# Performance work log

Hardware: AMD Instinct MI355X
Metric: run time of the kernel (lower is better)

## Reference

```python
import jax, jax.numpy as jnp
import numpy as np

N = 20000          # nodes (= masked tokens M, node_ids = arange)
E = 320000         # edges
D_H = 256          # hidden_channels
D_Z = 256          # node_channels
D_A = 256          # attn_channels
D_M = 256          # mlp_hidden_channels
V = 512            # predictor vocab size


def setup_inputs() -> dict:
    key = jax.random.key(0)
    ks = jax.random.split(key, 10)

    def lin(k, fan_in, fan_out):
        return jax.random.normal(k, (fan_in, fan_out), jnp.float32) / np.sqrt(fan_in)

    h_mask = jax.random.normal(ks[0], (N, D_H), jnp.float32)
    z = jax.random.normal(ks[1], (N, D_Z), jnp.float32)
    edge_index = jax.random.randint(ks[2], (2, E), 0, N, dtype=jnp.int32)
    node_ids = jnp.arange(N, dtype=jnp.int32)
    # Pairing of (masked token, edge): with node_ids = arange(N), every edge's
    # dst is a masked node, so masked_idx = dst and edge_idx = arange(E).
    masked_idx = edge_index[1]
    edge_idx = jnp.arange(E, dtype=jnp.int32)
    return {
        "h_mask": h_mask,
        "z": z,
        "Wq": lin(ks[3], D_Z, D_A), "bq": jnp.zeros((D_A,), jnp.float32),
        "Wk": lin(ks[4], D_Z, D_A), "bk": jnp.zeros((D_A,), jnp.float32),
        "W1": lin(ks[5], D_Z, D_M), "b1": jnp.zeros((D_M,), jnp.float32),
        "W2": lin(ks[6], D_M, D_H), "b2": jnp.zeros((D_H,), jnp.float32),
        "Wpred": lin(ks[7], D_H, V), "bpred": jnp.zeros((V,), jnp.float32),
        "edge_index": edge_index,
        "node_ids": node_ids,
        "masked_idx": masked_idx,
        "edge_idx": edge_idx,
    }


def reference(h_mask, z, Wq, bq, Wk, bk, W1, b1, W2, b2, Wpred, bpred,
              edge_index, node_ids, masked_idx, edge_idx):
    src = edge_index[0]
    # Node-level projections (N x D), computed once then gathered per pair.
    q = z @ Wq + bq                      # [N, D_A]
    k = z @ Wk + bk                      # [N, D_A]

    center_nodes = jnp.take(node_ids, masked_idx, axis=0)   # [P]
    neighbor_nodes = jnp.take(src, edge_idx, axis=0)        # [P]

    q_i = jnp.take(q, center_nodes, axis=0)                 # [P, D_A]
    k_j = jnp.take(k, neighbor_nodes, axis=0)               # [P, D_A]
    a_ij = jax.nn.sigmoid(jnp.sum(q_i * k_j, axis=-1, keepdims=True))  # [P, 1]

    h_i = jnp.take(h_mask, masked_idx, axis=0)              # [P, D_H]
    z_j = jnp.take(z, neighbor_nodes, axis=0)               # [P, D_Z]
    g_zj = jax.nn.relu(z_j @ W1 + b1) @ W2 + b2             # [P, D_H]

    h_tilde = a_ij * h_i + (1.0 - a_ij) * g_zj              # [P, D_H]
    edge_logits = h_tilde @ Wpred + bpred                   # [P, V]
    return edge_logits, masked_idx
```

## Files before the change

### kernel.cpp

```cpp
#include <hip/hip_runtime.h>
#include <hip/hip_bf16.h>

typedef __attribute__((ext_vector_type(8))) short s16x8;
typedef __attribute__((ext_vector_type(4))) float f32x4;
typedef __attribute__((ext_vector_type(2))) float f32x2;

__device__ inline unsigned int f2bf(float f) {
    union { float f; unsigned int i; } v;
    v.f = f;
    return (v.i + 0x7FFFu + ((v.i >> 16) & 1u)) >> 16;
}
__device__ inline unsigned char f2fp8(float v) {
    const int p = __builtin_amdgcn_cvt_pk_fp8_f32(v, v, 0, false);
    return (unsigned char)(p & 0xFF);
}

__global__ __launch_bounds__(256) void prep_w(
    const float* __restrict__ Wq, const float* __restrict__ Wk,
    const float* __restrict__ W1, const float* __restrict__ W2,
    const float* __restrict__ Wp,
    const float* __restrict__ bq, const float* __restrict__ bk,
    const float* __restrict__ b1,
    unsigned short* __restrict__ Wtqkt, unsigned short* __restrict__ Wt2,
    unsigned short* __restrict__ Wtp, float* __restrict__ bqkt)
{
    const int tid = threadIdx.x;
    int b = blockIdx.x;
    if (b < 1024) {
        const int w = b >> 8;
        const int i = (b & 255) * 256 + tid;
        const int k = i >> 8, j = i & 255;
        const float* W = (w == 0) ? Wq : (w == 1) ? Wk : (w == 2) ? W1 : W2;
        unsigned short* dst = (w == 3) ? Wt2 : (Wtqkt + w * 65536);
        dst[j * 256 + k] = (unsigned short)f2bf(W[i]);
        return;
    }
    b -= 1024;
    if (b < 512) {
        const int i = b * 256 + tid;
        const int k = i >> 9, j = i & 511;
        Wtp[(size_t)j * 256 + k] = (unsigned short)f2bf(Wp[i]);
        return;
    }
    b -= 512;
    {
        const int i = b * 256 + tid;
        bqkt[i] = (i < 256) ? bq[i] : (i < 512) ? bk[i - 256] : b1[i - 512];
    }
}

struct GemmJob {
    const void* A;
    const unsigned short* Wt;
    const float* bias;
    void* out1;
    void* out2;
    int Nout;
    int split;
    int relu_lo, relu_hi;
    int a_f32;
    int fp8_1, fp8_2;
};

__device__ inline void job_store(const GemmJob& J, int row, int col, float v, int M) {
    if (row >= M) return;
    if (J.bias) v += J.bias[col];
    if (col >= J.relu_lo && col < J.relu_hi) v = fmaxf(v, 0.0f);
    const bool lo = (col < J.split);
    void* o = lo ? J.out1 : J.out2;
    const int stride = lo ? J.split : (J.Nout - J.split);
    const int cc = lo ? col : col - J.split;
    const int f8 = lo ? J.fp8_1 : J.fp8_2;
    if (f8) ((unsigned char*)o)[(size_t)row * stride + cc] = f2fp8(v);
    else    ((unsigned short*)o)[(size_t)row * stride + cc] = (unsigned short)f2bf(v);
}

__global__ __launch_bounds__(256) void gemm_multi(
    GemmJob j0, GemmJob j1, int M)
{
    __shared__ __align__(16) char smem[65536];
    char* ldsA = smem;
    char* ldsB = smem + 32768;
    const GemmJob J = (blockIdx.y == 0) ? j0 : j1;

    const int tid  = threadIdx.x;
    const int wid  = tid >> 6, lane = tid & 63;
    const int wr   = wid >> 1, wc = wid & 1;
    const int r0   = blockIdx.x * 64;
    const int swz  = (lane & 7) << 4;

    if (J.a_f32) {
        const float* Af = (const float*)J.A;
        for (int i = tid; i < 2048; i += 256) {
            const int row = i >> 5, off = i & 31;
            const int gr = r0 + row;
            uint4 v = make_uint4(0, 0, 0, 0);
            if (gr < M) {
                const float4 a = *(const float4*)(Af + (size_t)gr * 256 + off * 8);
                const float4 c = *(const float4*)(Af + (size_t)gr * 256 + off * 8 + 4);
                v.x = f2bf(a.x) | (f2bf(a.y) << 16);
                v.y = f2bf(a.z) | (f2bf(a.w) << 16);
                v.z = f2bf(c.x) | (f2bf(c.y) << 16);
                v.w = f2bf(c.z) | (f2bf(c.w) << 16);
            }
            const int b = (row * 512 + off * 16) ^ ((row & 7) << 4);
            *(uint4*)(ldsA + b) = v;
        }
    } else {
        const unsigned short* Ab = (const unsigned short*)J.A;
        for (int i = tid; i < 2048; i += 256) {
            const int row = i >> 5, off = i & 31;
            const int gr = r0 + row;
            uint4 v = make_uint4(0, 0, 0, 0);
            if (gr < M) v = *(const uint4*)(Ab + (size_t)gr * 256 + off * 8);
            const int b = (row * 512 + off * 16) ^ ((row & 7) << 4);
            *(uint4*)(ldsA + b) = v;
        }
    }

    const int ro = lane & 15, ko = (lane >> 4) * 16;
    const int baseA0 = (wr * 32 +  0 + ro) * 512 + ko;
    const int baseA1 = (wr * 32 + 16 + ro) * 512 + ko;
    const int baseB0 = (wc * 32 +  0 + ro) * 512 + ko;
    const int baseB1 = (wc * 32 + 16 + ro) * 512 + ko;

    const int nchunks = J.Nout >> 6;
    for (int c = 0; c < nchunks; ++c) {
        const int j0c = c << 6;
        for (int i = tid; i < 2048; i += 256) {
            const int row = i >> 5, off = i & 31;
            const uint4 v = *(const uint4*)(J.Wt + (size_t)(j0c + row) * 256 + off * 8);
            const int b = (row * 512 + off * 16) ^ ((row & 7) << 4);
            *(uint4*)(ldsB + b) = v;
        }
        __syncthreads();

        f32x4 acc00 = {0,0,0,0}, acc01 = {0,0,0,0}, acc10 = {0,0,0,0}, acc11 = {0,0,0,0};
#pragma unroll
        for (int kk = 0; kk < 8; ++kk) {
            const int kb = kk * 64;
            const s16x8 a0 = *(const s16x8*)(ldsA + ((baseA0 + kb) ^ swz));
            const s16x8 a1 = *(const s16x8*)(ldsA + ((baseA1 + kb) ^ swz));
            const s16x8 b0 = *(const s16x8*)(ldsB + ((baseB0 + kb) ^ swz));
            const s16x8 b1 = *(const s16x8*)(ldsB + ((baseB1 + kb) ^ swz));
            acc00 = __builtin_amdgcn_mfma_f32_16x16x32_bf16(a0, b0, acc00, 0, 0, 0);
            acc01 = __builtin_amdgcn_mfma_f32_16x16x32_bf16(a0, b1, acc01, 0, 0, 0);
            acc10 = __builtin_amdgcn_mfma_f32_16x16x32_bf16(a1, b0, acc10, 0, 0, 0);
            acc11 = __builtin_amdgcn_mfma_f32_16x16x32_bf16(a1, b1, acc11, 0, 0, 0);
        }

        const int colb = j0c + wc * 32;
        const int rb0 = r0 + wr * 32 + (lane >> 4) * 4;
        const int rb1 = rb0 + 16;
#pragma unroll
        for (int r = 0; r < 4; ++r) {
            job_store(J, rb0 + r, colb + ro,      acc00[r], M);
            job_store(J, rb0 + r, colb + 16 + ro, acc01[r], M);
            job_store(J, rb1 + r, colb + ro,      acc10[r], M);
            job_store(J, rb1 + r, colb + 16 + ro, acc11[r], M);
        }
        __syncthreads();
    }
}

__global__ __launch_bounds__(256) void edge_fused(
    const unsigned char* __restrict__ qkb,
    const unsigned char* __restrict__ hp, const unsigned char* __restrict__ gp,
    const float* __restrict__ bpred,
    const int* __restrict__ edge_src, const int* __restrict__ node_ids,
    const int* __restrict__ masked_idx, const int* __restrict__ edge_idx,
    float* __restrict__ out, int P)
{
    const int wave = threadIdx.x >> 6;
    const int lane = threadIdx.x & 63;
    const int e = blockIdx.x * 4 + wave;
    if (e >= P) return;

    const int mi = masked_idx[e];
    const int c  = node_ids[mi];
    const int s  = edge_src[edge_idx[e]];

    const unsigned int qw = *(const unsigned int*)(qkb + (size_t)c * 512 + lane * 4);
    const unsigned int kw = *(const unsigned int*)(qkb + (size_t)s * 512 + 256 + lane * 4);
    const f32x2 q01 = __builtin_amdgcn_cvt_pk_f32_fp8(qw, false);
    const f32x2 q23 = __builtin_amdgcn_cvt_pk_f32_fp8(qw, true);
    const f32x2 k01 = __builtin_amdgcn_cvt_pk_f32_fp8(kw, false);
    const f32x2 k23 = __builtin_amdgcn_cvt_pk_f32_fp8(kw, true);
    float dot = q01.x * k01.x + q01.y * k01.y + q23.x * k23.x + q23.y * k23.y;
#pragma unroll
    for (int off = 32; off; off >>= 1) dot += __shfl_xor(dot, off, 64);

    const float a = 1.0f / (1.0f + expf(-dot));
    const float oma = 1.0f - a;

    const uint2 hv = *(const uint2*)(hp + (size_t)c * 512 + lane * 8);
    const uint2 gv = *(const uint2*)(gp + (size_t)s * 512 + lane * 8);
    const float4 bp0 = *(const float4*)&bpred[lane * 8];
    const float4 bp1 = *(const float4*)&bpred[lane * 8 + 4];

    const f32x2 h0 = __builtin_amdgcn_cvt_pk_f32_fp8(hv.x, false);
    const f32x2 h1 = __builtin_amdgcn_cvt_pk_f32_fp8(hv.x, true);
    const f32x2 h2 = __builtin_amdgcn_cvt_pk_f32_fp8(hv.y, false);
    const f32x2 h3 = __builtin_amdgcn_cvt_pk_f32_fp8(hv.y, true);
    const f32x2 g0 = __builtin_amdgcn_cvt_pk_f32_fp8(gv.x, false);
    const f32x2 g1 = __builtin_amdgcn_cvt_pk_f32_fp8(gv.x, true);
    const f32x2 g2 = __builtin_amdgcn_cvt_pk_f32_fp8(gv.y, false);
    const f32x2 g3 = __builtin_amdgcn_cvt_pk_f32_fp8(gv.y, true);

    float4 r0, r1;
    r0.x = fmaf(a, h0.x, fmaf(oma, g0.x, bp0.x));
    r0.y = fmaf(a, h0.y, fmaf(oma, g0.y, bp0.y));
    r0.z = fmaf(a, h1.x, fmaf(oma, g1.x, bp0.z));
    r0.w = fmaf(a, h1.y, fmaf(oma, g1.y, bp0.w));
    r1.x = fmaf(a, h2.x, fmaf(oma, g2.x, bp1.x));
    r1.y = fmaf(a, h2.y, fmaf(oma, g2.y, bp1.y));
    r1.z = fmaf(a, h3.x, fmaf(oma, g3.x, bp1.z));
    r1.w = fmaf(a, h3.y, fmaf(oma, g3.y, bp1.w));

    float* dst = &out[(size_t)e * 512 + lane * 8];
    *(float4*)(dst)     = r0;
    *(float4*)(dst + 4) = r1;

    if (lane == 0) {
        out[(size_t)P * 512 + e] = (float)mi;
    }
}

extern "C" void kernel_launch(void* const* d_in, const int* in_sizes, int n_in,
                              void* d_out, int out_size, void* d_ws, size_t ws_size,
                              hipStream_t stream) {
    const float* h_mask = (const float*)d_in[0];
    const float* z      = (const float*)d_in[1];
    const float* Wq     = (const float*)d_in[2];
    const float* bq     = (const float*)d_in[3];
    const float* Wk     = (const float*)d_in[4];
    const float* bk     = (const float*)d_in[5];
    const float* W1     = (const float*)d_in[6];
    const float* b1     = (const float*)d_in[7];
    const float* W2     = (const float*)d_in[8];
    const float* b2     = (const float*)d_in[9];
    const float* Wpred  = (const float*)d_in[10];
    const float* bpred  = (const float*)d_in[11];
    const int* edge_index = (const int*)d_in[12];
    const int* node_ids   = (const int*)d_in[13];
    const int* masked_idx = (const int*)d_in[14];
    const int* edge_idx   = (const int*)d_in[15];

    const int N = in_sizes[13];
    const int P = in_sizes[14];

    unsigned char*  qkb   = (unsigned char*)d_ws;
    unsigned char*  gpb   = qkb + (size_t)N * 512;
    unsigned char*  hpb   = gpb + (size_t)N * 512;
    unsigned short* tb    = (unsigned short*)(hpb + (size_t)N * 512);
    unsigned short* gb    = tb  + (size_t)N * 256;
    unsigned short* Wtqkt = gb  + (size_t)N * 256;
    unsigned short* Wt2   = Wtqkt + 196608;
    unsigned short* Wtp   = Wt2   + 65536;
    float*          bqkt  = (float*)(Wtp + 131072);

    const dim3 blk(256);
    const int gb64 = (N + 63) / 64;
    const int eb   = (P + 3) / 4;

    prep_w<<<dim3(1024 + 512 + 3), blk, 0, stream>>>(
        Wq, Wk, W1, W2, Wpred, bq, bk, b1, Wtqkt, Wt2, Wtp, bqkt);

    GemmJob a0 = { z,      Wtqkt, bqkt,    qkb, tb,      768, 512, 512, 768, 1, 1, 0 };
    GemmJob a1 = { h_mask, Wtp,   nullptr, hpb, nullptr, 512, 512, 0,   0,   1, 1, 0 };
    gemm_multi<<<dim3(gb64, 2), blk, 0, stream>>>(a0, a1, N);

    GemmJob b0 = { tb, Wt2, b2, gb, nullptr, 256, 256, 0, 0, 0, 0, 0 };
    gemm_multi<<<dim3(gb64, 1), blk, 0, stream>>>(b0, b0, N);

    GemmJob c0 = { gb, Wtp, nullptr, gpb, nullptr, 512, 512, 0, 0, 0, 1, 0 };
    gemm_multi<<<dim3(gb64, 1), blk, 0, stream>>>(c0, c0, N);

    edge_fused<<<dim3(eb), blk, 0, stream>>>(qkb, hpb, gpb, bpred,
                                             edge_index, node_ids, masked_idx, edge_idx,
                                             (float*)d_out, P);
}
```

Measured before the change: 349.4 us.

## Process 64 edges per wave with double-buffered gathers and nontemporal stores

The edge kernel now gives each wave a run of 64 edges instead of one. Indices are loaded once per lane and broadcast with shuffles, and the gather loads for the next edge are issued before the current edge is computed, so two edges are in flight. Output stores use nontemporal hints, and the masked_idx tail is written coalesced. The launch has 64x fewer blocks, which lowers occupancy and memory-level parallelism on the store-bound output path.

```diff
diff --git a/kernel.cpp b/kernel.cpp
--- a/kernel.cpp
+++ b/kernel.cpp
@@ -163,7 +163,7 @@
     }
 }
 
-__global__ __launch_bounds__(256) void edge_fused(
+__global__ __launch_bounds__(256) void edge_fused_v2(
     const unsigned char* __restrict__ qkb,
     const unsigned char* __restrict__ hp, const unsigned char* __restrict__ gp,
     const float* __restrict__ bpred,
@@ -171,58 +171,81 @@
     const int* __restrict__ masked_idx, const int* __restrict__ edge_idx,
     float* __restrict__ out, int P)
 {
-    const int wave = threadIdx.x >> 6;
-    const int lane = threadIdx.x & 63;
-    const int e = blockIdx.x * 4 + wave;
-    if (e >= P) return;
-
-    const int mi = masked_idx[e];
-    const int c  = node_ids[mi];
-    const int s  = edge_src[edge_idx[e]];
-
-    const unsigned int qw = *(const unsigned int*)(qkb + (size_t)c * 512 + lane * 4);
-    const unsigned int kw = *(const unsigned int*)(qkb + (size_t)s * 512 + 256 + lane * 4);
-    const f32x2 q01 = __builtin_amdgcn_cvt_pk_f32_fp8(qw, false);
-    const f32x2 q23 = __builtin_amdgcn_cvt_pk_f32_fp8(qw, true);
-    const f32x2 k01 = __builtin_amdgcn_cvt_pk_f32_fp8(kw, false);
-    const f32x2 k23 = __builtin_amdgcn_cvt_pk_f32_fp8(kw, true);
-    float dot = q01.x * k01.x + q01.y * k01.y + q23.x * k23.x + q23.y * k23.y;
-#pragma unroll
-    for (int off = 32; off; off >>= 1) dot += __shfl_xor(dot, off, 64);
-
-    const float a = 1.0f / (1.0f + expf(-dot));
-    const float oma = 1.0f - a;
-
-    const uint2 hv = *(const uint2*)(hp + (size_t)c * 512 + lane * 8);
-    const uint2 gv = *(const uint2*)(gp + (size_t)s * 512 + lane * 8);
+    const int wid  = threadIdx.x >> 6, lane = threadIdx.x & 63;
+    const int ebase = (blockIdx.x * 4 + wid) * 64;
+    if (ebase >= P) return;
+    const int ne = min(64, P - ebase);
+
+    int mi = 0, c = 0, s = 0;
+    if (lane < ne) {
+        mi = masked_idx[ebase + lane];
+        c  = node_ids[mi];
+        s  = edge_src[edge_idx[ebase + lane]];
+    }
+    if (lane < ne) out[(size_t)P * 512 + ebase + lane] = (float)mi;
+
     const float4 bp0 = *(const float4*)&bpred[lane * 8];
     const float4 bp1 = *(const float4*)&bpred[lane * 8 + 4];
 
-    const f32x2 h0 = __builtin_amdgcn_cvt_pk_f32_fp8(hv.x, false);
-    const f32x2 h1 = __builtin_amdgcn_cvt_pk_f32_fp8(hv.x, true);
-    const f32x2 h2 = __builtin_amdgcn_cvt_pk_f32_fp8(hv.y, false);
-    const f32x2 h3 = __builtin_amdgcn_cvt_pk_f32_fp8(hv.y, true);
-    const f32x2 g0 = __builtin_amdgcn_cvt_pk_f32_fp8(gv.x, false);
-    const f32x2 g1 = __builtin_amdgcn_cvt_pk_f32_fp8(gv.x, true);
-    const f32x2 g2 = __builtin_amdgcn_cvt_pk_f32_fp8(gv.y, false);
-    const f32x2 g3 = __builtin_amdgcn_cvt_pk_f32_fp8(gv.y, true);
-
-    float4 r0, r1;
-    r0.x = fmaf(a, h0.x, fmaf(oma, g0.x, bp0.x));
-    r0.y = fmaf(a, h0.y, fmaf(oma, g0.y, bp0.y));
-    r0.z = fmaf(a, h1.x, fmaf(oma, g1.x, bp0.z));
-    r0.w = fmaf(a, h1.y, fmaf(oma, g1.y, bp0.w));
-    r1.x = fmaf(a, h2.x, fmaf(oma, g2.x, bp1.x));
-    r1.y = fmaf(a, h2.y, fmaf(oma, g2.y, bp1.y));
-    r1.z = fmaf(a, h3.x, fmaf(oma, g3.x, bp1.z));
-    r1.w = fmaf(a, h3.y, fmaf(oma, g3.y, bp1.w));
-
-    float* dst = &out[(size_t)e * 512 + lane * 8];
-    *(float4*)(dst)     = r0;
-    *(float4*)(dst + 4) = r1;
-
-    if (lane == 0) {
-        out[(size_t)P * 512 + e] = (float)mi;
+    auto issue = [&](int j, unsigned int& qw, unsigned int& kw, uint2& hv, uint2& gv) {
+        const int cj = __shfl(c, j, 64);
+        const int sj = __shfl(s, j, 64);
+        qw = *(const unsigned int*)(qkb + (size_t)cj * 512 + lane * 4);
+        kw = *(const unsigned int*)(qkb + (size_t)sj * 512 + 256 + lane * 4);
+        hv = *(const uint2*)(hp + (size_t)cj * 512 + lane * 8);
+        gv = *(const uint2*)(gp + (size_t)sj * 512 + lane * 8);
+    };
+    auto do_edge = [&](int j, unsigned int qw, unsigned int kw, uint2 hv, uint2 gv) {
+        const f32x2 q01 = __builtin_amdgcn_cvt_pk_f32_fp8(qw, false);
+        const f32x2 q23 = __builtin_amdgcn_cvt_pk_f32_fp8(qw, true);
+        const f32x2 k01 = __builtin_amdgcn_cvt_pk_f32_fp8(kw, false);
+        const f32x2 k23 = __builtin_amdgcn_cvt_pk_f32_fp8(kw, true);
+        float dot = q01.x * k01.x + q01.y * k01.y + q23.x * k23.x + q23.y * k23.y;
+#pragma unroll
+        for (int off = 32; off; off >>= 1) dot += __shfl_xor(dot, off, 64);
+        const float a = 1.0f / (1.0f + expf(-dot));
+        const float oma = 1.0f - a;
+
+        const f32x2 h0 = __builtin_amdgcn_cvt_pk_f32_fp8(hv.x, false);
+        const f32x2 h1 = __builtin_amdgcn_cvt_pk_f32_fp8(hv.x, true);
+        const f32x2 h2 = __builtin_amdgcn_cvt_pk_f32_fp8(hv.y, false);
+        const f32x2 h3 = __builtin_amdgcn_cvt_pk_f32_fp8(hv.y, true);
+        const f32x2 g0 = __builtin_amdgcn_cvt_pk_f32_fp8(gv.x, false);
+        const f32x2 g1 = __builtin_amdgcn_cvt_pk_f32_fp8(gv.x, true);
+        const f32x2 g2 = __builtin_amdgcn_cvt_pk_f32_fp8(gv.y, false);
+        const f32x2 g3 = __builtin_amdgcn_cvt_pk_f32_fp8(gv.y, true);
+
+        f32x4 r0, r1;
+        r0[0] = fmaf(a, h0.x, fmaf(oma, g0.x, bp0.x));
+        r0[1] = fmaf(a, h0.y, fmaf(oma, g0.y, bp0.y));
+        r0[2] = fmaf(a, h1.x, fmaf(oma, g1.x, bp0.z));
+        r0[3] = fmaf(a, h1.y, fmaf(oma, g1.y, bp0.w));
+        r1[0] = fmaf(a, h2.x, fmaf(oma, g2.x, bp1.x));
+        r1[1] = fmaf(a, h2.y, fmaf(oma, g2.y, bp1.y));
+        r1[2] = fmaf(a, h3.x, fmaf(oma, g3.x, bp1.z));
+        r1[3] = fmaf(a, h3.y, fmaf(oma, g3.y, bp1.w));
+
+        float* dst = &out[(size_t)(ebase + j) * 512 + lane * 8];
+        __builtin_nontemporal_store(r0, (f32x4*)dst);
+        __builtin_nontemporal_store(r1, (f32x4*)(dst + 4));
+    };
+
+    unsigned int qA, kA; uint2 hA, gA;
+    unsigned int qB, kB; uint2 hB, gB;
+
+    if (ne == 64) {
+        issue(0, qA, kA, hA, gA);
+        for (int j = 0; j < 64; j += 2) {
+            issue(j + 1, qB, kB, hB, gB);
+            do_edge(j, qA, kA, hA, gA);
+            if (j + 2 < 64) issue(j + 2, qA, kA, hA, gA);
+            do_edge(j + 1, qB, kB, hB, gB);
+        }
+    } else {
+        for (int j = 0; j < ne; ++j) {
+            issue(j, qA, kA, hA, gA);
+            do_edge(j, qA, kA, hA, gA);
+        }
     }
 }
 
@@ -261,7 +284,7 @@
 
     const dim3 blk(256);
     const int gb64 = (N + 63) / 64;
-    const int eb   = (P + 3) / 4;
+    const int eb2  = (P + 255) / 256;
 
     prep_w<<<dim3(1024 + 512 + 3), blk, 0, stream>>>(
         Wq, Wk, W1, W2, Wpred, bq, bk, b1, Wtqkt, Wt2, Wtp, bqkt);
@@ -276,7 +299,7 @@
     GemmJob c0 = { gb, Wtp, nullptr, gpb, nullptr, 512, 512, 0, 0, 0, 1, 0 };
     gemm_multi<<<dim3(gb64, 1), blk, 0, stream>>>(c0, c0, N);
 
-    edge_fused<<<dim3(eb), blk, 0, stream>>>(qkb, hpb, gpb, bpred,
-                                             edge_index, node_ids, masked_idx, edge_idx,
-                                             (float*)d_out, P);
-}
+    edge_fused_v2<<<dim3(eb2), blk, 0, stream>>>(qkb, hpb, gpb, bpred,
+                                                 edge_index, node_ids, masked_idx, edge_idx,
+                                                 (float*)d_out, P);
+}
```

After: 398.9 us. 1.14x slower.
